# Kernel optimization log

Hardware: AMD Instinct MI355X
Metric: run time of the kernel (lower is better)

Reference implementation:

```python
import jax, jax.numpy as jnp
import numpy as np

N_QUBITS = 12
DIM = 2 ** N_QUBITS
BATCH = 2048


def setup_inputs() -> dict:
    key = jax.random.key(0)
    k1, k2, k3 = jax.random.split(key, 3)
    inputs = jax.random.normal(k1, (BATCH, N_QUBITS), dtype=jnp.float32)
    weight = jax.random.normal(k2, (3 + 2 * N_QUBITS,), dtype=jnp.float32)
    entangle_matrix = jax.random.normal(k3, (DIM, DIM), dtype=jnp.float32)
    return {"inputs": inputs, "weight": weight, "entangle_matrix": entangle_matrix}


def _encode(ry_angles, rz_angles):
    # Encoder: state = prod over qubits of first column of (Rz*Ry) per qubit.
    ry = ry_angles / 2
    rz = rz_angles / 2
    a = jnp.cos(ry) * jnp.exp(-1j * rz)  # entry11 (row bit = 0)
    b = jnp.sin(ry) * jnp.exp(1j * rz)   # entry21 (row bit = 1)
    col2 = jnp.stack([a, b], axis=-1).astype(jnp.complex64)  # [B, n, 2]
    B, n = ry.shape
    v = jnp.ones((B, 1), dtype=jnp.complex64)
    for q in range(n):  # Kronecker fold over qubits (big-endian, matches dec2bin)
        v = (v[:, :, None] * col2[:, q][:, None, :]).reshape(B, -1)
    return v  # [B, 2^n]


def _rot_mat(w):
    # rot_mat: per-qubit Rx(w[q]) @ Rz(w[n+q]), then full Kronecker product.
    n = w.shape[0] // 2
    tx = (w[:n] / 2).astype(jnp.complex64)
    tz = (w[n:] / 2).astype(jnp.complex64)
    c, s = jnp.cos(tx), jnp.sin(tx)
    rx = jnp.stack([jnp.stack([c, -1j * s], -1),
                    jnp.stack([-1j * s, c], -1)], -2)  # [n,2,2]
    ez = jnp.exp(-1j * tz)
    zero = jnp.zeros_like(ez)
    rz = jnp.stack([jnp.stack([ez, zero], -1),
                    jnp.stack([zero, jnp.exp(1j * tz)], -1)], -2)  # [n,2,2]
    mats = jnp.einsum('qij,qjk->qik', rx, rz)
    M = mats[0]
    for q in range(1, n):
        M = jnp.kron(M, mats[q])
    return M  # [2^n, 2^n]


def _ry2(theta):
    a = theta / 2
    c, s = jnp.cos(a), jnp.sin(a)
    return jnp.stack([jnp.stack([c, -s]), jnp.stack([s, c])])  # [2,2] real


def _final_rot(th3):
    # final_rot_mat: Rz-form @ Ry-form @ Rx-form (all ry_mat_list), kron with identity.
    rot = _ry2(th3[2]) @ (_ry2(th3[1]) @ _ry2(th3[0]))
    eye = jnp.eye(DIM // 2, dtype=jnp.complex64)
    return jnp.kron(rot.astype(jnp.complex64), eye)  # [DIM, DIM]


def reference(inputs, weight, entangle_matrix):
    # initial=False branch
    ry_angles = inputs
    rz_angles = jnp.square(inputs)
    v = _encode(ry_angles, rz_angles)                 # [B, DIM] complex64
    E = entangle_matrix.astype(jnp.complex64)
    R = _rot_mat(weight[3:])
    M = E @ R @ E                                     # [DIM, DIM]
    v = v @ M.T                                       # tensordot dims ([-1],[-1])
    F = _final_rot(weight[:3])
    v = v @ F.T
    half = DIM // 2
    # vector[:, half:] = 0 then sum |.|^2  <=>  sum over first half
    return jnp.sum(jnp.square(jnp.abs(v[:, :half])), axis=-1)  # [B] float32
```

## Files before the change

### kernel.cpp

```cpp
#include <hip/hip_runtime.h>
#include <math.h>

#define QDIM 4096
#define NQ 12
#define QBATCH 2048

typedef _Float16 f16x8 __attribute__((ext_vector_type(8)));
typedef float f32x4 __attribute__((ext_vector_type(4)));
typedef int i32x4 __attribute__((ext_vector_type(4)));

__device__ __forceinline__ void gld_lds16(const void* gptr, void* ldsptr) {
    __builtin_amdgcn_global_load_lds(
        (const __attribute__((address_space(1))) void*)gptr,
        (__attribute__((address_space(3))) void*)ldsptr,
        16, 0, 0);
}

__device__ __forceinline__ int q8(float x) {
    float y = fminf(fmaxf(x, -127.f), 127.f);
    return (int)rintf(y);
}
__device__ __forceinline__ int pack4_i8(int a, int b, int c, int d) {
    return (a & 0xFF) | ((b & 0xFF) << 8) | ((c & 0xFF) << 16) | ((d & 0xFF) << 24);
}

__global__ __launch_bounds__(256) void conv_kernel(
    const float* __restrict__ E, const float* __restrict__ wgt,
    _Float16* __restrict__ Eh, signed char* __restrict__ G8)
{
    float th = 0.5f * (wgt[0] + wgt[1] + wgt[2]);
    float c0 = cosf(th), c1 = -sinf(th);
    const float qs = 127.f / 6.f;
    size_t flat = ((size_t)blockIdx.x * 256 + threadIdx.x) * 8;
    size_t n = flat >> 12;
    size_t k = flat & (QDIM - 1);
    const float* p0 = E + n * QDIM + k;
    const float* p1 = p0 + (size_t)QBATCH * QDIM;
    float4 a0 = ((const float4*)p0)[0], a1 = ((const float4*)p0)[1];
    float4 b0 = ((const float4*)p1)[0], b1 = ((const float4*)p1)[1];
    f16x8 h0 = { (_Float16)a0.x, (_Float16)a0.y, (_Float16)a0.z, (_Float16)a0.w,
                 (_Float16)a1.x, (_Float16)a1.y, (_Float16)a1.z, (_Float16)a1.w };
    f16x8 h1 = { (_Float16)b0.x, (_Float16)b0.y, (_Float16)b0.z, (_Float16)b0.w,
                 (_Float16)b1.x, (_Float16)b1.y, (_Float16)b1.z, (_Float16)b1.w };
    *(f16x8*)&Eh[n * QDIM + k] = h0;
    *(f16x8*)&Eh[(n + QBATCH) * QDIM + k] = h1;
    float g[8] = { c0*a0.x + c1*b0.x, c0*a0.y + c1*b0.y, c0*a0.z + c1*b0.z, c0*a0.w + c1*b0.w,
                   c0*a1.x + c1*b1.x, c0*a1.y + c1*b1.y, c0*a1.z + c1*b1.z, c0*a1.w + c1*b1.w };
    int2 gp = { pack4_i8(q8(g[0]*qs), q8(g[1]*qs), q8(g[2]*qs), q8(g[3]*qs)),
                pack4_i8(q8(g[4]*qs), q8(g[5]*qs), q8(g[6]*qs), q8(g[7]*qs)) };
    *(int2*)&G8[n * QDIM + k] = gp;
}

__global__ __launch_bounds__(256) void expand_kernel(
    const float* __restrict__ inputs, _Float16* __restrict__ A1,
    float* __restrict__ out)
{
    __shared__ float ab[NQ][4];
    const int b = blockIdx.x;
    const int tid = threadIdx.x;
    if (tid == 0) out[b] = 0.f;
    if (tid < NQ) {
        float x = inputs[b * NQ + tid];
        float ry = 0.5f * x;
        float rz = 0.5f * x * x;
        float ca = cosf(ry), sa = sinf(ry), cz = cosf(rz), sz = sinf(rz);
        ab[tid][0] = ca * cz;  ab[tid][1] = -ca * sz;
        ab[tid][2] = sa * cz;  ab[tid][3] =  sa * sz;
    }
    __syncthreads();
    float pr0 = 1.f, pi0 = 0.f;
#pragma unroll
    for (int q = 0; q < 8; ++q) {
        int bit = (tid >> (7 - q)) & 1;
        float cr = ab[q][bit * 2 + 0], ci = ab[q][bit * 2 + 1];
        float nr = pr0 * cr - pi0 * ci;
        float ni = pr0 * ci + pi0 * cr;
        pr0 = nr; pi0 = ni;
    }
    f16x8 vr[2], vi[2];
#pragma unroll
    for (int u = 0; u < 16; ++u) {
        float pr = pr0, pi = pi0;
#pragma unroll
        for (int q = 8; q < 12; ++q) {
            int bit = (u >> (11 - q)) & 1;
            float cr = ab[q][bit * 2 + 0], ci = ab[q][bit * 2 + 1];
            float nr = pr * cr - pi * ci;
            float ni = pr * ci + pi * cr;
            pr = nr; pi = ni;
        }
        vr[u >> 3][u & 7] = (_Float16)pr;
        vi[u >> 3][u & 7] = (_Float16)pi;
    }
    const int idx0 = tid * 16;
    *(f16x8*)&A1[(size_t)b * QDIM + idx0] = vr[0];
    *(f16x8*)&A1[(size_t)b * QDIM + idx0 + 8] = vr[1];
    *(f16x8*)&A1[(size_t)(b + QBATCH) * QDIM + idx0] = vi[0];
    *(f16x8*)&A1[(size_t)(b + QBATCH) * QDIM + idx0 + 8] = vi[1];
}

#define VMCNT(N_) asm volatile("s_waitcnt vmcnt(" #N_ ")" ::: "memory")
#define LGKM0()   asm volatile("s_waitcnt lgkmcnt(0)" ::: "memory")
#define LGKM8()   asm volatile("s_waitcnt lgkmcnt(8)" ::: "memory")
#define SBAR()                              \
    do {                                    \
        asm volatile("" ::: "memory");      \
        __builtin_amdgcn_s_barrier();       \
        asm volatile("" ::: "memory");      \
    } while (0)

__global__ __launch_bounds__(512, 2) void gemm_f16_256(
    const _Float16* __restrict__ A, const _Float16* __restrict__ B,
    _Float16* __restrict__ C, int N)
{
    const int K = QDIM;
    __shared__ __attribute__((aligned(16))) _Float16 As[2][256 * 64];
    __shared__ __attribute__((aligned(16))) _Float16 Bs[2][256 * 64];

    const int tid  = threadIdx.x;
    const int wave = tid >> 6;
    const int lane = tid & 63;
    const int bm0 = blockIdx.y * 256;
    const int bn0 = blockIdx.x * 256;
    const int wm0 = (wave >> 2) * 128;
    const int wn0 = (wave & 3) * 64;
    const int q = lane >> 4;
    const int r = lane & 15;
    const int rx = r & 7;

    f32x4 acc[8][4];
#pragma unroll
    for (int i = 0; i < 8; ++i)
#pragma unroll
        for (int j = 0; j < 4; ++j) acc[i][j] = (f32x4){0.f, 0.f, 0.f, 0.f};

    const int srow = tid >> 3;
    const int scol = ((tid & 7) ^ (srow & 7)) * 8;
    const _Float16* gA = A + (size_t)(bm0 + srow) * K + scol;
    const _Float16* gB = B + (size_t)(bn0 + srow) * K + scol;

#define STG_A(D, KK, NN) gld_lds16(gA + (size_t)(NN) * 64 * K + (KK), &As[D][(NN) * 4096 + wave * 512])
#define STG_B(D, KK, NN) gld_lds16(gB + (size_t)(NN) * 64 * K + (KK), &Bs[D][(NN) * 4096 + wave * 512])
#define STG_AH(D, KK, H) do { STG_A(D, KK, 2*(H)); STG_A(D, KK, 2*(H)+1); } while (0)
#define STG_BH(D, KK, H) do { STG_B(D, KK, 2*(H)); STG_B(D, KK, 2*(H)+1); } while (0)

#define RD_A4(DST, D, IB)                                                          \
    _Pragma("unroll")                                                              \
    for (int ii = 0; ii < 4; ++ii) {                                               \
        _Pragma("unroll")                                                          \
        for (int ss = 0; ss < 2; ++ss)                                             \
            DST[ii][ss] = *(const f16x8*)&As[D][(wm0 + ((IB) + ii) * 16 + r) * 64  \
                                                + (((ss * 4 + q) ^ rx) * 8)];      \
    }
#define RD_B2(DST, D, JB)                                                          \
    _Pragma("unroll")                                                              \
    for (int jj = 0; jj < 2; ++jj) {                                               \
        _Pragma("unroll")                                                          \
        for (int ss = 0; ss < 2; ++ss)                                             \
            DST[jj][ss] = *(const f16x8*)&Bs[D][(wn0 + ((JB) + jj) * 16 + r) * 64  \
                                                + (((ss * 4 + q) ^ rx) * 8)];      \
    }
#define MM8(AR, BR, I0, J0)                                                        \
    _Pragma("unroll")                                                              \
    for (int ii = 0; ii < 4; ++ii) {                                               \
        _Pragma("unroll")                                                          \
        for (int jj = 0; jj < 2; ++jj) {                                           \
            acc[(I0) + ii][(J0) + jj] = __builtin_amdgcn_mfma_f32_16x16x32_f16(    \
                AR[ii][0], BR[jj][0], acc[(I0) + ii][(J0) + jj], 0, 0, 0);         \
            acc[(I0) + ii][(J0) + jj] = __builtin_amdgcn_mfma_f32_16x16x32_f16(    \
                AR[ii][1], BR[jj][1], acc[(I0) + ii][(J0) + jj], 0, 0, 0);         \
        }                                                                          \
    }

    f16x8 a0[4][2], a1[4][2], b0[2][2], b1[2][2];

    STG_AH(0, 0, 0); STG_AH(0, 0, 1);
    STG_BH(0, 0, 0); STG_BH(0, 0, 1);
    STG_BH(1, 64, 0); STG_BH(1, 64, 1);
    VMCNT(4);
    SBAR();

    for (int tau = 0; tau < 32; ++tau) {
        const int k1 = (2 * tau + 1) * 64;
        const int k2 = ((2 * tau + 2) & 63) * 64;
        const int k3 = ((2 * tau + 3) & 63) * 64;

        RD_A4(a0, 0, 0); RD_B2(b0, 0, 0);
        STG_AH(1, k1, 0);
        LGKM8();
        SBAR(); LGKM0();
        __builtin_amdgcn_s_setprio(1);
        MM8(a0, b0, 0, 0);
        __builtin_amdgcn_s_setprio(0);
        SBAR();

        RD_B2(b1, 0, 2);
        STG_AH(1, k1, 1);
        SBAR(); LGKM0();
        __builtin_amdgcn_s_setprio(1);
        MM8(a0, b1, 0, 2);
        __builtin_amdgcn_s_setprio(0);
        SBAR();

        RD_A4(a1, 0, 4);
        STG_BH(0, k2, 0);
        SBAR(); LGKM0();
        __builtin_amdgcn_s_setprio(1);
        MM8(a1, b1, 4, 2);
        __builtin_amdgcn_s_setprio(0);
        SBAR();

        STG_BH(0, k2, 1);
        VMCNT(4);
        SBAR(); LGKM0();
        __builtin_amdgcn_s_setprio(1);
        MM8(a1, b0, 4, 0);
        __builtin_amdgcn_s_setprio(0);
        SBAR();

        RD_A4(a0, 1, 0); RD_B2(b0, 1, 0);
        STG_AH(0, k2, 0);
        LGKM8();
        SBAR(); LGKM0();
        __builtin_amdgcn_s_setprio(1);
        MM8(a0, b0, 0, 0);
        __builtin_amdgcn_s_setprio(0);
        SBAR();

        RD_B2(b1, 1, 2);
        STG_AH(0, k2, 1);
        SBAR(); LGKM0();
        __builtin_amdgcn_s_setprio(1);
        MM8(a0, b1, 0, 2);
        __builtin_amdgcn_s_setprio(0);
        SBAR();

        RD_A4(a1, 1, 4);
        STG_BH(1, k3, 0);
        SBAR(); LGKM0();
        __builtin_amdgcn_s_setprio(1);
        MM8(a1, b1, 4, 2);
        __builtin_amdgcn_s_setprio(0);
        SBAR();

        STG_BH(1, k3, 1);
        VMCNT(4);
        SBAR(); LGKM0();
        __builtin_amdgcn_s_setprio(1);
        MM8(a1, b0, 4, 0);
        __builtin_amdgcn_s_setprio(0);
        SBAR();
    }
    VMCNT(0);

#pragma unroll
    for (int i = 0; i < 8; ++i) {
        const int crow = bm0 + wm0 + i * 16 + q * 4;
#pragma unroll
        for (int rr = 0; rr < 4; ++rr)
#pragma unroll
            for (int j = 0; j < 4; ++j)
                C[(size_t)(crow + rr) * N + bn0 + wn0 + j * 16 + r] = (_Float16)acc[i][j][rr];
    }
#undef STG_A
#undef STG_B
#undef STG_AH
#undef STG_BH
#undef RD_A4
#undef RD_B2
#undef MM8
}

__global__ __launch_bounds__(256) void butterfly_kernel(
    const _Float16* __restrict__ u1, const float* __restrict__ wgt,
    signed char* __restrict__ A2, float* __restrict__ scaleA)
{
    __shared__ float sRe[4366];
    __shared__ float sIm[4366];
    __shared__ float mats[NQ][8];
    __shared__ float red[8];
    const int blk = blockIdx.x;
    const int tid = threadIdx.x;
    const int ah = tid >> 4;
    const int al = tid & 15;

    if (tid < NQ) {
        float tx = 0.5f * wgt[3 + tid];
        float tz = 0.5f * wgt[15 + tid];
        float c = cosf(tx), s = sinf(tx), cz = cosf(tz), sz = sinf(tz);
        mats[tid][0] =  c * cz;  mats[tid][1] = -c * sz;
        mats[tid][2] =  s * sz;  mats[tid][3] = -s * cz;
        mats[tid][4] = -s * sz;  mats[tid][5] = -s * cz;
        mats[tid][6] =  c * cz;  mats[tid][7] =  c * sz;
    }

    float xr[16], xi[16];
    {
        const _Float16* pRe = u1 + (size_t)blk * QDIM + tid * 16;
        const _Float16* pIm = u1 + (size_t)(blk + QBATCH) * QDIM + tid * 16;
        f16x8 r0 = ((const f16x8*)pRe)[0], r1 = ((const f16x8*)pRe)[1];
        f16x8 i0 = ((const f16x8*)pIm)[0], i1 = ((const f16x8*)pIm)[1];
#pragma unroll
        for (int j = 0; j < 8; ++j) {
            xr[j] = (float)r0[j]; xr[8 + j] = (float)r1[j];
            xi[j] = (float)i0[j]; xi[8 + j] = (float)i1[j];
        }
    }
    __syncthreads();

#define BFLY_STAGE(arrR, arrI, K_, Q_)                                         \
    {                                                                          \
        const float m00r = mats[Q_][0], m00i = mats[Q_][1];                    \
        const float m01r = mats[Q_][2], m01i = mats[Q_][3];                    \
        const float m10r = mats[Q_][4], m10i = mats[Q_][5];                    \
        const float m11r = mats[Q_][6], m11i = mats[Q_][7];                    \
        _Pragma("unroll")                                                      \
        for (int t = 0; t < 8; ++t) {                                          \
            int i0 = ((t >> (K_)) << ((K_) + 1)) | (t & ((1 << (K_)) - 1));    \
            int i1 = i0 | (1 << (K_));                                         \
            float x0r = arrR[i0], x0i = arrI[i0];                              \
            float x1r = arrR[i1], x1i = arrI[i1];                              \
            arrR[i0] = m00r * x0r - m00i * x0i + m01r * x1r - m01i * x1i;      \
            arrI[i0] = m00r * x0i + m00i * x0r + m01r * x1i + m01i * x1r;      \
            arrR[i1] = m10r * x0r - m10i * x0i + m11r * x1r - m11i * x1i;      \
            arrI[i1] = m10r * x0i + m10i * x0r + m11r * x1i + m11i * x1r;      \
        }                                                                      \
    }

#pragma unroll
    for (int p = 0; p < 4; ++p) BFLY_STAGE(xr, xi, p, 11 - p);

#pragma unroll
    for (int c = 0; c < 16; ++c) {
        sRe[273 * ah + 17 * al + c] = xr[c];
        sIm[273 * ah + 17 * al + c] = xi[c];
    }
    __syncthreads();

    float yr[16], yi[16];
#pragma unroll
    for (int b = 0; b < 16; ++b) {
        yr[b] = sRe[273 * ah + 17 * b + al];
        yi[b] = sIm[273 * ah + 17 * b + al];
    }
#pragma unroll
    for (int p = 0; p < 4; ++p) BFLY_STAGE(yr, yi, p, 7 - p);

#pragma unroll
    for (int b = 0; b < 16; ++b) {
        sRe[273 * ah + 17 * b + al] = yr[b];
        sIm[273 * ah + 17 * b + al] = yi[b];
    }
    __syncthreads();

    float zr[16], zi[16];
#pragma unroll
    for (int a = 0; a < 16; ++a) {
        zr[a] = sRe[273 * a + 17 * ah + al];
        zi[a] = sIm[273 * a + 17 * ah + al];
    }
#pragma unroll
    for (int p = 0; p < 4; ++p) BFLY_STAGE(zr, zi, p, 3 - p);

    float mR = 0.f, mI = 0.f;
#pragma unroll
    for (int j = 0; j < 16; ++j) {
        mR = fmaxf(mR, fabsf(zr[j]));
        mI = fmaxf(mI, fabsf(zi[j]));
    }
#pragma unroll
    for (int off = 32; off > 0; off >>= 1) {
        mR = fmaxf(mR, __shfl_xor(mR, off, 64));
        mI = fmaxf(mI, __shfl_xor(mI, off, 64));
    }
    const int wid = tid >> 6;
    if ((tid & 63) == 0) { red[wid] = mR; red[4 + wid] = mI; }
    __syncthreads();
    mR = fmaxf(fmaxf(red[0], red[1]), fmaxf(red[2], red[3]));
    mI = fmaxf(fmaxf(red[4], red[5]), fmaxf(red[6], red[7]));
    mR = fmaxf(mR, 1e-30f);
    mI = fmaxf(mI, 1e-30f);
    if (tid == 0) {
        scaleA[blk] = mR / 127.f;
        scaleA[blk + QBATCH] = mI / 127.f;
    }
    const float invR = 127.f / mR, invI = 127.f / mI;

    signed char* oRe = A2 + (size_t)blk * QDIM + ah * 16 + al;
    signed char* oIm = A2 + (size_t)(blk + QBATCH) * QDIM + ah * 16 + al;
#pragma unroll
    for (int a = 0; a < 16; ++a) {
        oRe[a * 256] = (signed char)q8(zr[a] * invR);
        oIm[a * 256] = (signed char)q8(zi[a] * invI);
    }
#undef BFLY_STAGE
}

__global__ __launch_bounds__(512, 2) void gemm2_i8_256(
    const signed char* __restrict__ A, const signed char* __restrict__ B,
    const float* __restrict__ scaleA, float* __restrict__ out)
{
    const int K = QDIM;
    __shared__ __attribute__((aligned(16))) signed char As[2][256 * 128];
    __shared__ __attribute__((aligned(16))) signed char Bs[2][128 * 128];

    const int tid  = threadIdx.x;
    const int wave = tid >> 6;
    const int lane = tid & 63;
    const int bn0 = blockIdx.x * 128;
    const int bm0 = blockIdx.y * 256;
    const int wm0 = (wave >> 1) * 64;
    const int wn0 = (wave & 1) * 64;
    const int q = lane >> 4;
    const int r = lane & 15;
    const int rx = r & 7;

    i32x4 acc[4][4];
#pragma unroll
    for (int i = 0; i < 4; ++i)
#pragma unroll
        for (int j = 0; j < 4; ++j) acc[i][j] = (i32x4){0, 0, 0, 0};

    const int srow = tid >> 3;
    const int scol = ((tid & 7) ^ (srow & 7)) * 16;
    const signed char* gA = A + (size_t)(bm0 + srow) * K + scol;
    const signed char* gB = B + (size_t)(bn0 + srow) * K + scol;

#define STG2_A(D, KK, NN) gld_lds16(gA + (size_t)(NN) * 64 * K + (KK), &As[D][(NN) * 8192 + wave * 1024])
#define STG2_B(D, KK, NN) gld_lds16(gB + (size_t)(NN) * 64 * K + (KK), &Bs[D][(NN) * 8192 + wave * 1024])

#define RD2_A(DST, D, IB)                                                           \
    _Pragma("unroll")                                                               \
    for (int ii = 0; ii < 2; ++ii) {                                                \
        _Pragma("unroll")                                                           \
        for (int ss = 0; ss < 2; ++ss)                                              \
            DST[ii][ss] = *(const i32x4*)&As[D][(wm0 + ((IB) + ii) * 16 + r) * 128  \
                                                + (((ss * 4 + q) ^ rx) * 16)];      \
    }
#define RD2_B(DST, D, JB)                                                           \
    _Pragma("unroll")                                                               \
    for (int jj = 0; jj < 2; ++jj) {                                                \
        _Pragma("unroll")                                                           \
        for (int ss = 0; ss < 2; ++ss)                                              \
            DST[jj][ss] = *(const i32x4*)&Bs[D][(wn0 + ((JB) + jj) * 16 + r) * 128  \
                                                + (((ss * 4 + q) ^ rx) * 16)];      \
    }
#define MM2(AR, BR, I0, J0)                                                         \
    _Pragma("unroll")                                                               \
    for (int ii = 0; ii < 2; ++ii) {                                                \
        _Pragma("unroll")                                                           \
        for (int jj = 0; jj < 2; ++jj) {                                            \
            acc[(I0) + ii][(J0) + jj] = __builtin_amdgcn_mfma_i32_16x16x64_i8(      \
                AR[ii][0], BR[jj][0], acc[(I0) + ii][(J0) + jj], 0, 0, 0);          \
            acc[(I0) + ii][(J0) + jj] = __builtin_amdgcn_mfma_i32_16x16x64_i8(      \
                AR[ii][1], BR[jj][1], acc[(I0) + ii][(J0) + jj], 0, 0, 0);          \
        }                                                                           \
    }

    i32x4 a0[2][2], a1[2][2], b0[2][2], b1[2][2];

    STG2_B(0, 0, 0); STG2_B(0, 0, 1);
    STG2_A(0, 0, 0); STG2_A(0, 0, 1); STG2_A(0, 0, 2); STG2_A(0, 0, 3);
    STG2_B(1, 128, 0); STG2_B(1, 128, 1);
    VMCNT(2);
    SBAR();

    for (int tau = 0; tau < 16; ++tau) {
        const int k1 = (2 * tau + 1) * 128;
        const int k2 = ((2 * tau + 2) & 31) * 128;
        const int k3 = ((2 * tau + 3) & 31) * 128;

        RD2_A(a0, 0, 0); RD2_B(b0, 0, 0);
        STG2_A(1, k1, 0); STG2_A(1, k1, 1);
        SBAR(); LGKM0();
        __builtin_amdgcn_s_setprio(1);
        MM2(a0, b0, 0, 0);
        __builtin_amdgcn_s_setprio(0);
        SBAR();

        RD2_B(b1, 0, 2);
        STG2_A(1, k1, 2); STG2_A(1, k1, 3);
        SBAR(); LGKM0();
        __builtin_amdgcn_s_setprio(1);
        MM2(a0, b1, 0, 2);
        __builtin_amdgcn_s_setprio(0);
        SBAR();

        RD2_A(a1, 0, 2);
        SBAR(); LGKM0();
        __builtin_amdgcn_s_setprio(1);
        MM2(a1, b1, 2, 2);
        __builtin_amdgcn_s_setprio(0);
        SBAR();

        STG2_B(0, k2, 0); STG2_B(0, k2, 1);
        VMCNT(2);
        SBAR(); LGKM0();
        __builtin_amdgcn_s_setprio(1);
        MM2(a1, b0, 2, 0);
        __builtin_amdgcn_s_setprio(0);
        SBAR();

        RD2_A(a0, 1, 0); RD2_B(b0, 1, 0);
        STG2_A(0, k2, 0); STG2_A(0, k2, 1);
        SBAR(); LGKM0();
        __builtin_amdgcn_s_setprio(1);
        MM2(a0, b0, 0, 0);
        __builtin_amdgcn_s_setprio(0);
        SBAR();

        RD2_B(b1, 1, 2);
        STG2_A(0, k2, 2); STG2_A(0, k2, 3);
        SBAR(); LGKM0();
        __builtin_amdgcn_s_setprio(1);
        MM2(a0, b1, 0, 2);
        __builtin_amdgcn_s_setprio(0);
        SBAR();

        RD2_A(a1, 1, 2);
        SBAR(); LGKM0();
        __builtin_amdgcn_s_setprio(1);
        MM2(a1, b1, 2, 2);
        __builtin_amdgcn_s_setprio(0);
        SBAR();

        STG2_B(1, k3, 0); STG2_B(1, k3, 1);
        VMCNT(2);
        SBAR(); LGKM0();
        __builtin_amdgcn_s_setprio(1);
        MM2(a1, b0, 2, 0);
        __builtin_amdgcn_s_setprio(0);
        SBAR();
    }
    VMCNT(0);

    const float dqG = 6.f / 127.f;
#pragma unroll
    for (int i = 0; i < 4; ++i) {
#pragma unroll
        for (int rr = 0; rr < 4; ++rr) {
            const int row = bm0 + wm0 + i * 16 + q * 4 + rr;
            const float sc = scaleA[row] * dqG;
            float v = 0.f;
#pragma unroll
            for (int j = 0; j < 4; ++j) {
                float t = sc * (float)acc[i][j][rr];
                v = fmaf(t, t, v);
            }
            v += __shfl_xor(v, 1, 64);
            v += __shfl_xor(v, 2, 64);
            v += __shfl_xor(v, 4, 64);
            v += __shfl_xor(v, 8, 64);
            if (r == 0) atomicAdd(&out[row & (QBATCH - 1)], v);
        }
    }
#undef STG2_A
#undef STG2_B
#undef RD2_A
#undef RD2_B
#undef MM2
}

extern "C" void kernel_launch(void* const* d_in, const int* in_sizes, int n_in,
                              void* d_out, int out_size, void* d_ws, size_t ws_size,
                              hipStream_t stream)
{
    const float* inputs = (const float*)d_in[0];
    const float* weight = (const float*)d_in[1];
    const float* E      = (const float*)d_in[2];
    float* out = (float*)d_out;

    char* ws = (char*)d_ws;
    const size_t MB = 1024 * 1024;
    _Float16*    Eh     = (_Float16*)   (ws + 0);
    signed char* G8     = (signed char*)(ws + 32 * MB);
    _Float16*    A1     = (_Float16*)   (ws + 40 * MB);
    _Float16*    u1     = (_Float16*)   (ws + 72 * MB);
    signed char* A2     = (signed char*)(ws + 104 * MB);
    float*       scaleA = (float*)      (ws + 120 * MB);

    conv_kernel<<<(QBATCH * QDIM / 8) / 256, 256, 0, stream>>>(E, weight, Eh, G8);
    expand_kernel<<<QBATCH, 256, 0, stream>>>(inputs, A1, out);
    gemm_f16_256<<<dim3(QDIM / 256, QDIM / 256), 512, 0, stream>>>(A1, Eh, u1, QDIM);
    butterfly_kernel<<<QBATCH, 256, 0, stream>>>(u1, weight, A2, scaleA);
    gemm2_i8_256<<<dim3(2048 / 128, QDIM / 256), 512, 0, stream>>>(A2, G8, scaleA, out);
}
```

Before: 298.1 us.

## Merge GEMM main-loop phases to halve barrier count per iteration

Restructures the pipelined fp16 MFMA main loop so each phase issues both LDS fragment reads and both global-to-LDS stage halves together, then runs two MM8 blocks before one barrier. The loop goes from eight barrier-separated phases to four, cutting s_barrier and lgkmcnt waits. In exchange, more register fragments are live at once, and the larger groups of in-flight loads could change latency hiding or stress the VMCNT(4) accounting, which was tuned for the old issue order.

```diff
diff --git a/kernel.cpp b/kernel.cpp
--- a/kernel.cpp
+++ b/kernel.cpp
@@ -185,68 +185,42 @@
         const int k2 = ((2 * tau + 2) & 63) * 64;
         const int k3 = ((2 * tau + 3) & 63) * 64;
 
-        RD_A4(a0, 0, 0); RD_B2(b0, 0, 0);
-        STG_AH(1, k1, 0);
+        RD_A4(a0, 0, 0); RD_B2(b0, 0, 0); RD_B2(b1, 0, 2);
+        STG_AH(1, k1, 0); STG_AH(1, k1, 1);
         LGKM8();
         SBAR(); LGKM0();
         __builtin_amdgcn_s_setprio(1);
         MM8(a0, b0, 0, 0);
-        __builtin_amdgcn_s_setprio(0);
-        SBAR();
-
-        RD_B2(b1, 0, 2);
-        STG_AH(1, k1, 1);
-        SBAR(); LGKM0();
-        __builtin_amdgcn_s_setprio(1);
         MM8(a0, b1, 0, 2);
         __builtin_amdgcn_s_setprio(0);
         SBAR();
 
         RD_A4(a1, 0, 4);
-        STG_BH(0, k2, 0);
+        STG_BH(0, k2, 0); STG_BH(0, k2, 1);
+        VMCNT(4);
         SBAR(); LGKM0();
         __builtin_amdgcn_s_setprio(1);
         MM8(a1, b1, 4, 2);
-        __builtin_amdgcn_s_setprio(0);
-        SBAR();
-
-        STG_BH(0, k2, 1);
+        MM8(a1, b0, 4, 0);
+        __builtin_amdgcn_s_setprio(0);
+        SBAR();
+
+        RD_A4(a0, 1, 0); RD_B2(b0, 1, 0); RD_B2(b1, 1, 2);
+        STG_AH(0, k2, 0); STG_AH(0, k2, 1);
+        LGKM8();
+        SBAR(); LGKM0();
+        __builtin_amdgcn_s_setprio(1);
+        MM8(a0, b0, 0, 0);
+        MM8(a0, b1, 0, 2);
+        __builtin_amdgcn_s_setprio(0);
+        SBAR();
+
+        RD_A4(a1, 1, 4);
+        STG_BH(1, k3, 0); STG_BH(1, k3, 1);
         VMCNT(4);
         SBAR(); LGKM0();
         __builtin_amdgcn_s_setprio(1);
-        MM8(a1, b0, 4, 0);
-        __builtin_amdgcn_s_setprio(0);
-        SBAR();
-
-        RD_A4(a0, 1, 0); RD_B2(b0, 1, 0);
-        STG_AH(0, k2, 0);
-        LGKM8();
-        SBAR(); LGKM0();
-        __builtin_amdgcn_s_setprio(1);
-        MM8(a0, b0, 0, 0);
-        __builtin_amdgcn_s_setprio(0);
-        SBAR();
-
-        RD_B2(b1, 1, 2);
-        STG_AH(0, k2, 1);
-        SBAR(); LGKM0();
-        __builtin_amdgcn_s_setprio(1);
-        MM8(a0, b1, 0, 2);
-        __builtin_amdgcn_s_setprio(0);
-        SBAR();
-
-        RD_A4(a1, 1, 4);
-        STG_BH(1, k3, 0);
-        SBAR(); LGKM0();
-        __builtin_amdgcn_s_setprio(1);
         MM8(a1, b1, 4, 2);
-        __builtin_amdgcn_s_setprio(0);
-        SBAR();
-
-        STG_BH(1, k3, 1);
-        VMCNT(4);
-        SBAR(); LGKM0();
-        __builtin_amdgcn_s_setprio(1);
         MM8(a1, b0, 4, 0);
         __builtin_amdgcn_s_setprio(0);
         SBAR();
```

Result: no change. 300.8 us (+0.9%).
